# Kernel tuning notes

Hardware: AMD Instinct MI355X
Metric: run time of the kernel (lower is better)

The kernel has to match this reference:

```python
import jax, jax.numpy as jnp
import numpy as np

B, T, U, NOUT = 64, 512, 256, 4


def lstm(x, W, Uh, b):
    """Keras-style LSTM. x: [B,T,F]. Returns (seq [B,T,U], last [B,U]).
    Gate order i, f, g(candidate), o; sigmoid recurrent activation, tanh activation."""
    xz = jnp.einsum('btf,fg->btg', x, W) + b  # precompute input projections [B,T,4U]

    def step(carry, xz_t):
        h, c = carry
        z = xz_t + h @ Uh
        i, f, g, o = jnp.split(z, 4, axis=-1)
        i = jax.nn.sigmoid(i)
        f = jax.nn.sigmoid(f)
        g = jnp.tanh(g)
        o = jax.nn.sigmoid(o)
        c = f * c + i * g
        h = o * jnp.tanh(c)
        return (h, c), h

    h0 = jnp.zeros((x.shape[0], Uh.shape[0]), x.dtype)
    (h_last, _), hs = jax.lax.scan(step, (h0, h0), jnp.swapaxes(xz, 0, 1))
    return jnp.swapaxes(hs, 0, 1), h_last


def setup_inputs() -> dict:
    key = jax.random.key(0)
    ks = jax.random.split(key, 7)
    s_in = 1.0 / np.sqrt(U)
    return {
        'x': jax.random.normal(ks[0], (B, T, U), jnp.float32),
        'Wr': jax.random.normal(ks[1], (U, 4 * U), jnp.float32) * s_in,
        'Ur': jax.random.normal(ks[2], (U, 4 * U), jnp.float32) * s_in,
        'br': jnp.zeros((4 * U,), jnp.float32),
        'Wn': jax.random.normal(ks[3], (U, 4 * U), jnp.float32) * s_in,
        'Un': jax.random.normal(ks[4], (U, 4 * U), jnp.float32) * s_in,
        'bn': jnp.zeros((4 * U,), jnp.float32),
        'Wd': jax.random.normal(ks[5], (T * U, NOUT), jnp.float32) * (1.0 / np.sqrt(T * U)),
        'bd': jnp.zeros((NOUT,), jnp.float32),
    }


def reference(x, Wr, Ur, br, Wn, Un, bn, Wd, bd):
    # n_hidden = 3, inference (training=False): noise/dropout are identity.
    # Layer 0: shared return-sequences LSTM, no residual.
    h0, _ = lstm(x, Wr, Ur, br)                      # [B,T,U]
    # Layer 1: SAME shared LSTM weights, residual add.
    h1, _ = lstm(h0, Wr, Ur, br)
    h1 = h1 + h0                                     # [B,T,U]
    # Layer 2 (last): non-returning LSTM; residual Add broadcasts [B,U] + [B,T,U].
    _, h2 = lstm(h1, Wn, Un, bn)                     # [B,U]
    y = h2[:, None, :] + h1                          # [B,T,U]
    y = y.reshape(y.shape[0], -1)                    # flatten -> [B, T*U]
    return y @ Wd + bd                               # [B, NOUT]
```

## Files before the change

kernel.cpp:

```cpp
#include <hip/hip_runtime.h>
#include <hip/hip_fp16.h>
#include <cstddef>
#include <cstdint>

#define U_DIM 256
#define G_DIM 1024
#define T_DIM 512
#define B_DIM 64
#define TC    32
#define LOG2TC 5
#define NCHUNK (T_DIM / TC)
#define NSLOT  (NCHUNK + 2)
#define BHID   (B_DIM * U_DIM)
#define NPART  8

#define NG_TOT 32
#define NG_REG 23
#define NG_LDS 9

#if __has_builtin(__builtin_amdgcn_global_load_lds)
#define HAS_GLL 1
#else
#define HAS_GLL 0
#endif

typedef _Float16 half2v __attribute__((ext_vector_type(2)));
typedef _Float16 f16x8  __attribute__((ext_vector_type(8)));
typedef float    f32x4  __attribute__((ext_vector_type(4)));

__device__ __forceinline__ float fsig(float x) {
    return 1.0f / (1.0f + __expf(-x));
}
__device__ __forceinline__ float ftanh(float x) {
    return 2.0f * fsig(2.0f * x) - 1.0f;
}

#define PIN4(v) asm("" : "+v"(v.x), "+v"(v.y), "+v"(v.z), "+v"(v.w))

__global__ __launch_bounds__(256)
void pack_w(const float* __restrict__ U, uint4* __restrict__ P)
{
    const int idx = blockIdx.x * 256 + threadIdx.x;
    const int g = idx >> 10;
    const int n = idx & 1023;
    uint vals[4];
    #pragma unroll
    for (int j = 0; j < 4; ++j) {
        const int k = g * 8 + j * 2;
        const __half a = __float2half_rn(U[(size_t)k * G_DIM + n]);
        const __half b = __float2half_rn(U[(size_t)(k + 1) * G_DIM + n]);
        const unsigned short ua = __builtin_bit_cast(unsigned short, a);
        const unsigned short ub = __builtin_bit_cast(unsigned short, b);
        vals[j] = (uint)ua | ((uint)ub << 16);
    }
    P[idx] = make_uint4(vals[0], vals[1], vals[2], vals[3]);
}

__global__ __launch_bounds__(256)
void pack_x(const float* __restrict__ x, __half* __restrict__ xh)
{
    const size_t i = ((size_t)blockIdx.x * 256 + threadIdx.x) * 8;
    const float4 a = *(const float4*)(x + i);
    const float4 b = *(const float4*)(x + i + 4);
    ushort4 o0, o1;
    o0.x = __builtin_bit_cast(unsigned short, __float2half_rn(a.x));
    o0.y = __builtin_bit_cast(unsigned short, __float2half_rn(a.y));
    o0.z = __builtin_bit_cast(unsigned short, __float2half_rn(a.z));
    o0.w = __builtin_bit_cast(unsigned short, __float2half_rn(a.w));
    o1.x = __builtin_bit_cast(unsigned short, __float2half_rn(b.x));
    o1.y = __builtin_bit_cast(unsigned short, __float2half_rn(b.y));
    o1.z = __builtin_bit_cast(unsigned short, __float2half_rn(b.z));
    o1.w = __builtin_bit_cast(unsigned short, __float2half_rn(b.w));
    *(ushort4*)(xh + i) = o0;
    *(ushort4*)(xh + i + 4) = o1;
}

__device__ __forceinline__ float mac8(float acc, uint4 w, uint4 h)
{
#if __has_builtin(__builtin_amdgcn_fdot2)
    acc = __builtin_amdgcn_fdot2(__builtin_bit_cast(half2v, h.x),
                                 __builtin_bit_cast(half2v, w.x), acc, false);
    acc = __builtin_amdgcn_fdot2(__builtin_bit_cast(half2v, h.y),
                                 __builtin_bit_cast(half2v, w.y), acc, false);
    acc = __builtin_amdgcn_fdot2(__builtin_bit_cast(half2v, h.z),
                                 __builtin_bit_cast(half2v, w.z), acc, false);
    acc = __builtin_amdgcn_fdot2(__builtin_bit_cast(half2v, h.w),
                                 __builtin_bit_cast(half2v, w.w), acc, false);
#else
    const uint wv[4] = {w.x, w.y, w.z, w.w};
    const uint hv[4] = {h.x, h.y, h.z, h.w};
    #pragma unroll
    for (int j = 0; j < 4; ++j) {
        const __half2 wp = __builtin_bit_cast(__half2, wv[j]);
        const __half2 hp = __builtin_bit_cast(__half2, hv[j]);
        acc += __half2float(hp.x) * __half2float(wp.x);
        acc += __half2float(hp.y) * __half2float(wp.y);
    }
#endif
    return acc;
}

__global__
__attribute__((amdgpu_flat_work_group_size(512, 512)))
__attribute__((amdgpu_waves_per_eu(2, 2)))
void lstm_pipe(int slot,
               const __half* __restrict__ xzAll,
               const uint4* __restrict__ Pr, const uint4* __restrict__ Pn,
               __half* __restrict__ h0, __half* __restrict__ h1,
               float* __restrict__ hsAll, float* __restrict__ csAll)
{
    const int layer = blockIdx.x >> 6;
    const int b     = blockIdx.x & 63;
    const int c     = slot - layer;
    if ((unsigned)c >= (unsigned)NCHUNK) return;
    const int t0 = c * TC;

    const uint4* __restrict__ P = (layer < 2) ? Pr : Pn;
    const __half* __restrict__ xzb =
        xzAll + (size_t)layer * (B_DIM * TC * G_DIM) + (size_t)b * TC * G_DIM;
    const __half* __restrict__ resb =
        (layer == 1) ? (h0 + (size_t)(b * T_DIM + t0) * U_DIM) : nullptr;
    __half* __restrict__ outb =
        (layer == 0) ? (h0 + (size_t)(b * T_DIM + t0) * U_DIM)
      : (layer == 1) ? (h1 + (size_t)(b * T_DIM + t0) * U_DIM) : nullptr;
    float* __restrict__ hstate = hsAll + (size_t)layer * BHID + b * U_DIM;
    float* __restrict__ cstate = csAll + (size_t)layer * BHID + b * U_DIM;

    const int t = threadIdx.x;
    const int n0 = t;
    const int n1 = t + 512;

    __shared__ __align__(16) uint hq[U_DIM / 2];
    __shared__ float csh[U_DIM];
    __shared__ float zsh[G_DIM];
    __shared__ uint4 wlds[NG_LDS][G_DIM];

#if HAS_GLL
    {
        const int wbase = t & ~63;
        #pragma unroll
        for (int g = 0; g < NG_LDS; ++g) {
            __builtin_amdgcn_global_load_lds(
                (const __attribute__((address_space(1))) void*)
                    (P + (size_t)(NG_REG + g) * G_DIM + n0),
                (__attribute__((address_space(3))) void*)&wlds[g][wbase],
                16, 0, 0);
            __builtin_amdgcn_global_load_lds(
                (const __attribute__((address_space(1))) void*)
                    (P + (size_t)(NG_REG + g) * G_DIM + n1),
                (__attribute__((address_space(3))) void*)&wlds[g][512 + wbase],
                16, 0, 0);
        }
    }
#else
    #pragma unroll
    for (int g = 0; g < NG_LDS; ++g) {
        wlds[g][n0] = P[(size_t)(NG_REG + g) * G_DIM + n0];
        wlds[g][n1] = P[(size_t)(NG_REG + g) * G_DIM + n1];
    }
#endif

    if (t < U_DIM) {
        float hv, cv;
        if (c == 0) { hv = 0.0f; cv = 0.0f; }
        else        { hv = hstate[t]; cv = cstate[t]; }
        csh[t] = cv;
        ((__half*)hq)[t] = __float2half_rn(hv);
    }

    uint4 wA[NG_REG], wB[NG_REG];
    #pragma unroll
    for (int g = 0; g < NG_REG; ++g) {
        wA[g] = P[(size_t)g * G_DIM + n0];
        wB[g] = P[(size_t)g * G_DIM + n1];
    }
    #pragma unroll
    for (int g = 0; g < NG_REG; ++g) { PIN4(wA[g]); PIN4(wB[g]); }

    __syncthreads();

    float cur0 = __half2float(xzb[n0]);
    float cur1 = __half2float(xzb[n1]);
    float resv = (resb && t < U_DIM) ? __half2float(resb[t]) : 0.0f;

    for (int tl = 0; tl < TC; ++tl) {
        float acc0 = cur0;
        float acc1 = cur1;

        const int tn = (tl + 1 < TC) ? (tl + 1) : (TC - 1);
        cur0 = __half2float(xzb[(size_t)tn * G_DIM + n0]);
        cur1 = __half2float(xzb[(size_t)tn * G_DIM + n1]);
        const float resn = (resb && t < U_DIM)
                         ? __half2float(resb[(size_t)tn * U_DIM + t]) : 0.0f;

        const uint4* __restrict__ hp = (const uint4*)hq;

        #pragma unroll
        for (int g = 0; g < NG_REG; ++g) {
            const uint4 h4 = hp[g];
            acc0 = mac8(acc0, wA[g], h4);
            acc1 = mac8(acc1, wB[g], h4);
        }
        #pragma unroll
        for (int g = 0; g < NG_LDS; ++g) {
            const uint4 h4 = hp[NG_REG + g];
            acc0 = mac8(acc0, wlds[g][n0], h4);
            acc1 = mac8(acc1, wlds[g][n1], h4);
        }

        zsh[n0] = fsig(acc0);
        zsh[n1] = (t < U_DIM) ? ftanh(acc1) : fsig(acc1);
        __syncthreads();

        if (t < U_DIM) {
            const float iv = zsh[t];
            const float fv = zsh[t + 256];
            const float gv = zsh[t + 512];
            const float ov = zsh[t + 768];
            const float cc = fv * csh[t] + iv * gv;
            const float hh = ov * ftanh(cc);
            csh[t] = cc;
            ((__half*)hq)[t] = __float2half_rn(hh);
            if (outb) outb[(size_t)tl * U_DIM + t] = __float2half_rn(hh + resv);
        }
        resv = resn;
        __syncthreads();
    }

    if (t < U_DIM) {
        hstate[t] = __half2float(((const __half*)hq)[t]);
        cstate[t] = csh[t];
    }
}

__global__ __launch_bounds__(256)
void gemm3_mfma(int slot,
                const __half* __restrict__ xh,
                const __half* __restrict__ h0, const __half* __restrict__ h1,
                const uint4* __restrict__ PWr, const uint4* __restrict__ PWn,
                const float* __restrict__ br, const float* __restrict__ bn,
                __half* __restrict__ xzAll)
{
    const int z = blockIdx.z;
    const int c = slot - z;
    if ((unsigned)c >= (unsigned)NCHUNK) return;
    const int t0 = c * TC;

    const __half* __restrict__ A = (z == 0) ? xh : ((z == 1) ? h0 : h1);
    const uint4*  __restrict__ PW = (z < 2) ? PWr : PWn;
    const float*  __restrict__ bias = (z < 2) ? br : bn;
    __half* __restrict__ out = xzAll + (size_t)z * (B_DIM * TC * G_DIM);

    const int tid = threadIdx.x;
    const int w = tid >> 6;
    const int l = tid & 63;

    const int bm = blockIdx.y * 64;
    const int bn_ = blockIdx.x * 64;
    const int col = bn_ + w * 16 + (l & 15);
    const int krow = l >> 4;

    __shared__ __half ctile[64][68];

    const __half* arow[4];
    #pragma unroll
    for (int rt = 0; rt < 4; ++rt) {
        const int m = bm + rt * 16 + (l & 15);
        const int b = m >> LOG2TC;
        const int tl = m & (TC - 1);
        arow[rt] = A + (size_t)(b * T_DIM + t0 + tl) * U_DIM + krow * 8;
    }

    f32x4 acc[4] = {{0,0,0,0},{0,0,0,0},{0,0,0,0},{0,0,0,0}};

    #pragma unroll
    for (int kt = 0; kt < 8; ++kt) {
        const uint4 bfrag = PW[(size_t)(4 * kt + krow) * G_DIM + col];
        #pragma unroll
        for (int rt = 0; rt < 4; ++rt) {
            const uint4 afrag = *(const uint4*)(arow[rt] + kt * 32);
            acc[rt] = __builtin_amdgcn_mfma_f32_16x16x32_f16(
                __builtin_bit_cast(f16x8, afrag), __builtin_bit_cast(f16x8, bfrag),
                acc[rt], 0, 0, 0);
        }
    }

    const float bv = bias[col];
    const int ccol = w * 16 + (l & 15);
    #pragma unroll
    for (int rt = 0; rt < 4; ++rt) {
        #pragma unroll
        for (int r = 0; r < 4; ++r) {
            const int crow = rt * 16 + 4 * (l >> 4) + r;
            ctile[crow][ccol] = __float2half_rn(acc[rt][r] + bv);
        }
    }
    __syncthreads();

    {
        const int row = tid >> 2;
        const int quad = (tid & 3) * 16;
        const int m = bm + row;
        const int b = m >> LOG2TC;
        const int tl = m & (TC - 1);
        __half* dst = out + (size_t)(b * TC + tl) * G_DIM + bn_ + quad;
        const uint4 v0 = *(const uint4*)&ctile[row][quad];
        const uint4 v1 = *(const uint4*)&ctile[row][quad + 8];
        *(uint4*)dst = v0;
        *(uint4*)(dst + 8) = v1;
    }
}

__global__ __launch_bounds__(256)
void final_partial(const __half* __restrict__ h1, const float* __restrict__ h2,
                   const float* __restrict__ Wd, float* __restrict__ partials)
{
    const int b = blockIdx.x;
    const int p = blockIdx.y;
    const int tid = threadIdx.x;
    const int JTOT = T_DIM * U_DIM;
    const int JPART = JTOT / NPART;

    const __half* hb = h1 + (size_t)b * JTOT;
    const float* h2b = h2 + (size_t)b * U_DIM;

    float a0 = 0.f, a1 = 0.f, a2 = 0.f, a3 = 0.f;

    for (int j = p * JPART + tid * 8; j < (p + 1) * JPART; j += 256 * 8) {
        const uint4 hv = *(const uint4*)(hb + j);
        const int m = j & (U_DIM - 1);
        const float4 s0 = *(const float4*)(h2b + m);
        const float4 s1 = *(const float4*)(h2b + m + 4);
        float v[8];
        {
            const __half2 p0 = __builtin_bit_cast(__half2, hv.x);
            const __half2 p1 = __builtin_bit_cast(__half2, hv.y);
            const __half2 p2 = __builtin_bit_cast(__half2, hv.z);
            const __half2 p3 = __builtin_bit_cast(__half2, hv.w);
            v[0] = __half2float(p0.x) + s0.x;
            v[1] = __half2float(p0.y) + s0.y;
            v[2] = __half2float(p1.x) + s0.z;
            v[3] = __half2float(p1.y) + s0.w;
            v[4] = __half2float(p2.x) + s1.x;
            v[5] = __half2float(p2.y) + s1.y;
            v[6] = __half2float(p3.x) + s1.z;
            v[7] = __half2float(p3.y) + s1.w;
        }
        #pragma unroll
        for (int uu = 0; uu < 8; ++uu) {
            const float4 wv = *(const float4*)&Wd[(size_t)(j + uu) * 4];
            a0 += v[uu] * wv.x;
            a1 += v[uu] * wv.y;
            a2 += v[uu] * wv.z;
            a3 += v[uu] * wv.w;
        }
    }

    __shared__ float red[256][4];
    red[tid][0] = a0; red[tid][1] = a1; red[tid][2] = a2; red[tid][3] = a3;
    __syncthreads();
    for (int s = 128; s > 0; s >>= 1) {
        if (tid < s) {
            #pragma unroll
            for (int o = 0; o < 4; ++o) red[tid][o] += red[tid + s][o];
        }
        __syncthreads();
    }
    if (tid < 4) partials[((size_t)b * NPART + p) * 4 + tid] = red[0][tid];
}

__global__ __launch_bounds__(256)
void final_reduce(const float* __restrict__ partials, const float* __restrict__ bd,
                  float* __restrict__ y)
{
    const int tid = threadIdx.x;
    const int b = tid >> 2;
    const int o = tid & 3;
    float s = bd[o];
    #pragma unroll
    for (int p = 0; p < NPART; ++p)
        s += partials[((size_t)b * NPART + p) * 4 + o];
    y[b * 4 + o] = s;
}

extern "C" void kernel_launch(void* const* d_in, const int* in_sizes, int n_in,
                              void* d_out, int out_size, void* d_ws, size_t ws_size,
                              hipStream_t stream)
{
    (void)in_sizes; (void)n_in; (void)out_size; (void)ws_size;

    const float* x  = (const float*)d_in[0];
    const float* Wr = (const float*)d_in[1];
    const float* Ur = (const float*)d_in[2];
    const float* br = (const float*)d_in[3];
    const float* Wn = (const float*)d_in[4];
    const float* Un = (const float*)d_in[5];
    const float* bn = (const float*)d_in[6];
    const float* Wd = (const float*)d_in[7];
    const float* bd = (const float*)d_in[8];
    float* y = (float*)d_out;

    char* wp = (char*)d_ws;
    uint4* Pr  = (uint4*)wp;  wp += (size_t)NG_TOT * G_DIM * 16;
    uint4* Pn  = (uint4*)wp;  wp += (size_t)NG_TOT * G_DIM * 16;
    uint4* PWr = (uint4*)wp;  wp += (size_t)NG_TOT * G_DIM * 16;
    uint4* PWn = (uint4*)wp;  wp += (size_t)NG_TOT * G_DIM * 16;
    float* hsAll = (float*)wp;      wp += (size_t)3 * BHID * 4;
    float* csAll = (float*)wp;      wp += (size_t)3 * BHID * 4;
    float* partials = (float*)wp;   wp += (size_t)B_DIM * NPART * 4 * 4;
    wp = (char*)(((uintptr_t)wp + 255) & ~(uintptr_t)255);
    __half* xzAll = (__half*)wp; wp += (size_t)3 * B_DIM * TC * G_DIM * 2;
    __half* h0 = (__half*)wp;    wp += (size_t)B_DIM * T_DIM * U_DIM * 2;
    __half* h1 = (__half*)wp;    wp += (size_t)B_DIM * T_DIM * U_DIM * 2;
    __half* xh = (__half*)wp;    wp += (size_t)B_DIM * T_DIM * U_DIM * 2;

    pack_w<<<128, 256, 0, stream>>>(Ur, Pr);
    pack_w<<<128, 256, 0, stream>>>(Un, Pn);
    pack_w<<<128, 256, 0, stream>>>(Wr, PWr);
    pack_w<<<128, 256, 0, stream>>>(Wn, PWn);
    pack_x<<<(B_DIM * T_DIM * U_DIM) / (256 * 8), 256, 0, stream>>>(x, xh);

    dim3 ggrid(G_DIM / 64, (B_DIM * TC) / 64, 3);
    for (int slot = 0; slot < NSLOT; ++slot) {
        gemm3_mfma<<<ggrid, 256, 0, stream>>>(slot, xh, h0, h1, PWr, PWn,
                                              br, bn, xzAll);
        lstm_pipe<<<3 * B_DIM, 512, 0, stream>>>(slot, xzAll, Pr, Pn,
                                                 h0, h1, hsAll, csAll);
    }

    final_partial<<<dim3(B_DIM, NPART), 256, 0, stream>>>(h1, hsAll + 2 * BHID,
                                                          Wd, partials);
    final_reduce<<<1, 256, 0, stream>>>(partials, bd, y);
}
```

Baseline: 1.636 ms.

## Fuse next-chunk input projection GEMM into LSTM pipeline kernel with double-buffered xz

Removes the separate per-slot gemm3_mfma launch and instead has each lstm_pipe block compute, after its recurrent chunk, the input-projection tile that the following slot will consume (MFMA 16x16x32), written into a double-buffered xz workspace indexed by slot parity. Layer 2 blocks compute layer 0's next chunk of x projections. This halves the number of launches per slot and lets the projection work overlap with idle CUs. The risk is that the fused GEMM runs on only 192 blocks with B fragments read straight from global memory without LDS reuse, so it may be slower than the dedicated GEMM kernel. It also adds extra register pressure in a kernel pinned to two waves per EU.

```diff
diff --git a/kernel.cpp b/kernel.cpp
--- a/kernel.cpp
+++ b/kernel.cpp
@@ -100,31 +100,30 @@
     return acc;
 }
 
+#define XZ_TILE ((size_t)TC * G_DIM)
+#define XZ_AT(base, par, layer, b) \
+    ((base) + ((((size_t)(par) * 3 + (layer)) * B_DIM + (b)) * XZ_TILE))
+
 __global__
 __attribute__((amdgpu_flat_work_group_size(512, 512)))
 __attribute__((amdgpu_waves_per_eu(2, 2)))
 void lstm_pipe(int slot,
-               const __half* __restrict__ xzAll,
+               const __half* __restrict__ xh,
                const uint4* __restrict__ Pr, const uint4* __restrict__ Pn,
+               const uint4* __restrict__ PWr, const uint4* __restrict__ PWn,
+               const float* __restrict__ br, const float* __restrict__ bn,
                __half* __restrict__ h0, __half* __restrict__ h1,
+               __half* __restrict__ xzAll,
                float* __restrict__ hsAll, float* __restrict__ csAll)
 {
     const int layer = blockIdx.x >> 6;
     const int b     = blockIdx.x & 63;
     const int c     = slot - layer;
-    if ((unsigned)c >= (unsigned)NCHUNK) return;
-    const int t0 = c * TC;
-
-    const uint4* __restrict__ P = (layer < 2) ? Pr : Pn;
-    const __half* __restrict__ xzb =
-        xzAll + (size_t)layer * (B_DIM * TC * G_DIM) + (size_t)b * TC * G_DIM;
-    const __half* __restrict__ resb =
-        (layer == 1) ? (h0 + (size_t)(b * T_DIM + t0) * U_DIM) : nullptr;
-    __half* __restrict__ outb =
-        (layer == 0) ? (h0 + (size_t)(b * T_DIM + t0) * U_DIM)
-      : (layer == 1) ? (h1 + (size_t)(b * T_DIM + t0) * U_DIM) : nullptr;
-    float* __restrict__ hstate = hsAll + (size_t)layer * BHID + b * U_DIM;
-    float* __restrict__ cstate = csAll + (size_t)layer * BHID + b * U_DIM;
+    const bool do_lstm = (unsigned)c < (unsigned)NCHUNK;
+
+    const int cc = (layer == 2) ? (slot + 1) : (slot - layer);
+    const bool do_tail = (unsigned)cc < (unsigned)NCHUNK;
+    if (!do_lstm && !do_tail) return;
 
     const int t = threadIdx.x;
     const int n0 = t;
@@ -135,101 +134,164 @@
     __shared__ float zsh[G_DIM];
     __shared__ uint4 wlds[NG_LDS][G_DIM];
 
+    if (do_lstm) {
+        const int t0 = c * TC;
+        const uint4* __restrict__ P = (layer < 2) ? Pr : Pn;
+        const __half* __restrict__ xzb = XZ_AT(xzAll, slot & 1, layer, b);
+        const __half* __restrict__ resb =
+            (layer == 1) ? (h0 + (size_t)(b * T_DIM + t0) * U_DIM) : nullptr;
+        __half* __restrict__ outb =
+            (layer == 0) ? (h0 + (size_t)(b * T_DIM + t0) * U_DIM)
+          : (layer == 1) ? (h1 + (size_t)(b * T_DIM + t0) * U_DIM) : nullptr;
+        float* __restrict__ hstate = hsAll + (size_t)layer * BHID + b * U_DIM;
+        float* __restrict__ cstate = csAll + (size_t)layer * BHID + b * U_DIM;
+
 #if HAS_GLL
-    {
-        const int wbase = t & ~63;
+        {
+            const int wbase = t & ~63;
+            #pragma unroll
+            for (int g = 0; g < NG_LDS; ++g) {
+                __builtin_amdgcn_global_load_lds(
+                    (const __attribute__((address_space(1))) void*)
+                        (P + (size_t)(NG_REG + g) * G_DIM + n0),
+                    (__attribute__((address_space(3))) void*)&wlds[g][wbase],
+                    16, 0, 0);
+                __builtin_amdgcn_global_load_lds(
+                    (const __attribute__((address_space(1))) void*)
+                        (P + (size_t)(NG_REG + g) * G_DIM + n1),
+                    (__attribute__((address_space(3))) void*)&wlds[g][512 + wbase],
+                    16, 0, 0);
+            }
+        }
+#else
         #pragma unroll
         for (int g = 0; g < NG_LDS; ++g) {
-            __builtin_amdgcn_global_load_lds(
-                (const __attribute__((address_space(1))) void*)
-                    (P + (size_t)(NG_REG + g) * G_DIM + n0),
-                (__attribute__((address_space(3))) void*)&wlds[g][wbase],
-                16, 0, 0);
-            __builtin_amdgcn_global_load_lds(
-                (const __attribute__((address_space(1))) void*)
-                    (P + (size_t)(NG_REG + g) * G_DIM + n1),
-                (__attribute__((address_space(3))) void*)&wlds[g][512 + wbase],
-                16, 0, 0);
-        }
-    }
-#else
-    #pragma unroll
-    for (int g = 0; g < NG_LDS; ++g) {
-        wlds[g][n0] = P[(size_t)(NG_REG + g) * G_DIM + n0];
-        wlds[g][n1] = P[(size_t)(NG_REG + g) * G_DIM + n1];
-    }
+            wlds[g][n0] = P[(size_t)(NG_REG + g) * G_DIM + n0];
+            wlds[g][n1] = P[(size_t)(NG_REG + g) * G_DIM + n1];
+        }
 #endif
 
-    if (t < U_DIM) {
-        float hv, cv;
-        if (c == 0) { hv = 0.0f; cv = 0.0f; }
-        else        { hv = hstate[t]; cv = cstate[t]; }
-        csh[t] = cv;
-        ((__half*)hq)[t] = __float2half_rn(hv);
-    }
-
-    uint4 wA[NG_REG], wB[NG_REG];
-    #pragma unroll
-    for (int g = 0; g < NG_REG; ++g) {
-        wA[g] = P[(size_t)g * G_DIM + n0];
-        wB[g] = P[(size_t)g * G_DIM + n1];
-    }
-    #pragma unroll
-    for (int g = 0; g < NG_REG; ++g) { PIN4(wA[g]); PIN4(wB[g]); }
-
-    __syncthreads();
-
-    float cur0 = __half2float(xzb[n0]);
-    float cur1 = __half2float(xzb[n1]);
-    float resv = (resb && t < U_DIM) ? __half2float(resb[t]) : 0.0f;
-
-    for (int tl = 0; tl < TC; ++tl) {
-        float acc0 = cur0;
-        float acc1 = cur1;
-
-        const int tn = (tl + 1 < TC) ? (tl + 1) : (TC - 1);
-        cur0 = __half2float(xzb[(size_t)tn * G_DIM + n0]);
-        cur1 = __half2float(xzb[(size_t)tn * G_DIM + n1]);
-        const float resn = (resb && t < U_DIM)
-                         ? __half2float(resb[(size_t)tn * U_DIM + t]) : 0.0f;
-
-        const uint4* __restrict__ hp = (const uint4*)hq;
-
+        if (t < U_DIM) {
+            float hv, cv;
+            if (c == 0) { hv = 0.0f; cv = 0.0f; }
+            else        { hv = hstate[t]; cv = cstate[t]; }
+            csh[t] = cv;
+            ((__half*)hq)[t] = __float2half_rn(hv);
+        }
+
+        uint4 wA[NG_REG], wB[NG_REG];
         #pragma unroll
         for (int g = 0; g < NG_REG; ++g) {
-            const uint4 h4 = hp[g];
-            acc0 = mac8(acc0, wA[g], h4);
-            acc1 = mac8(acc1, wB[g], h4);
-        }
-        #pragma unroll
-        for (int g = 0; g < NG_LDS; ++g) {
-            const uint4 h4 = hp[NG_REG + g];
-            acc0 = mac8(acc0, wlds[g][n0], h4);
-            acc1 = mac8(acc1, wlds[g][n1], h4);
-        }
-
-        zsh[n0] = fsig(acc0);
-        zsh[n1] = (t < U_DIM) ? ftanh(acc1) : fsig(acc1);
+            wA[g] = P[(size_t)g * G_DIM + n0];
+            wB[g] = P[(size_t)g * G_DIM + n1];
+        }
+        #pragma unroll
+        for (int g = 0; g < NG_REG; ++g) { PIN4(wA[g]); PIN4(wB[g]); }
+
         __syncthreads();
 
+        float cur0 = __half2float(xzb[n0]);
+        float cur1 = __half2float(xzb[n1]);
+        float resv = (resb && t < U_DIM) ? __half2float(resb[t]) : 0.0f;
+
+        for (int tl = 0; tl < TC; ++tl) {
+            float acc0 = cur0;
+            float acc1 = cur1;
+
+            const int tn = (tl + 1 < TC) ? (tl + 1) : (TC - 1);
+            cur0 = __half2float(xzb[(size_t)tn * G_DIM + n0]);
+            cur1 = __half2float(xzb[(size_t)tn * G_DIM + n1]);
+            const float resn = (resb && t < U_DIM)
+                             ? __half2float(resb[(size_t)tn * U_DIM + t]) : 0.0f;
+
+            const uint4* __restrict__ hp = (const uint4*)hq;
+
+            #pragma unroll
+            for (int g = 0; g < NG_REG; ++g) {
+                const uint4 h4 = hp[g];
+                acc0 = mac8(acc0, wA[g], h4);
+                acc1 = mac8(acc1, wB[g], h4);
+            }
+            #pragma unroll
+            for (int g = 0; g < NG_LDS; ++g) {
+                const uint4 h4 = hp[NG_REG + g];
+                acc0 = mac8(acc0, wlds[g][n0], h4);
+                acc1 = mac8(acc1, wlds[g][n1], h4);
+            }
+
+            zsh[n0] = fsig(acc0);
+            zsh[n1] = (t < U_DIM) ? ftanh(acc1) : fsig(acc1);
+            __syncthreads();
+
+            if (t < U_DIM) {
+                const float iv = zsh[t];
+                const float fv = zsh[t + 256];
+                const float gv = zsh[t + 512];
+                const float ov = zsh[t + 768];
+                const float cc2 = fv * csh[t] + iv * gv;
+                const float hh = ov * ftanh(cc2);
+                csh[t] = cc2;
+                ((__half*)hq)[t] = __float2half_rn(hh);
+                if (outb) outb[(size_t)tl * U_DIM + t] = __float2half_rn(hh + resv);
+            }
+            resv = resn;
+            __syncthreads();
+        }
+
         if (t < U_DIM) {
-            const float iv = zsh[t];
-            const float fv = zsh[t + 256];
-            const float gv = zsh[t + 512];
-            const float ov = zsh[t + 768];
-            const float cc = fv * csh[t] + iv * gv;
-            const float hh = ov * ftanh(cc);
-            csh[t] = cc;
-            ((__half*)hq)[t] = __float2half_rn(hh);
-            if (outb) outb[(size_t)tl * U_DIM + t] = __float2half_rn(hh + resv);
-        }
-        resv = resn;
-        __syncthreads();
-    }
-
-    if (t < U_DIM) {
-        hstate[t] = __half2float(((const __half*)hq)[t]);
-        cstate[t] = csh[t];
+            hstate[t] = __half2float(((const __half*)hq)[t]);
+            cstate[t] = csh[t];
+        }
+    }
+
+    if (do_tail) {
+        const __half* __restrict__ asrc;
+        const uint4*  __restrict__ PW2;
+        const float*  __restrict__ bias2;
+        __half* __restrict__ xzo;
+        if (layer == 0) {
+            asrc = h0;  PW2 = PWr; bias2 = br;
+            xzo = XZ_AT(xzAll, (slot + 1) & 1, 1, b);
+        } else if (layer == 1) {
+            asrc = h1;  PW2 = PWn; bias2 = bn;
+            xzo = XZ_AT(xzAll, (slot + 1) & 1, 2, b);
+        } else {
+            asrc = xh;  PW2 = PWr; bias2 = br;
+            xzo = XZ_AT(xzAll, (slot + 1) & 1, 0, b);
+        }
+        const __half* arow0 =
+            asrc + (size_t)(b * T_DIM + cc * TC + (t & 15)) * U_DIM + ((t & 63) >> 4) * 8;
+        const __half* arow1 = arow0 + 16 * U_DIM;
+
+        const int w = t >> 6;
+        const int l = t & 63;
+        const int krow = l >> 4;
+
+        #pragma unroll
+        for (int ct = 0; ct < 8; ++ct) {
+            const int col = w * 128 + ct * 16 + (l & 15);
+            f32x4 acc0 = {0.f, 0.f, 0.f, 0.f};
+            f32x4 acc1 = {0.f, 0.f, 0.f, 0.f};
+            #pragma unroll
+            for (int kt = 0; kt < 8; ++kt) {
+                const uint4 bfrag = PW2[(size_t)(4 * kt + krow) * G_DIM + col];
+                const uint4 a0 = *(const uint4*)(arow0 + kt * 32);
+                const uint4 a1 = *(const uint4*)(arow1 + kt * 32);
+                acc0 = __builtin_amdgcn_mfma_f32_16x16x32_f16(
+                    __builtin_bit_cast(f16x8, a0), __builtin_bit_cast(f16x8, bfrag),
+                    acc0, 0, 0, 0);
+                acc1 = __builtin_amdgcn_mfma_f32_16x16x32_f16(
+                    __builtin_bit_cast(f16x8, a1), __builtin_bit_cast(f16x8, bfrag),
+                    acc1, 0, 0, 0);
+            }
+            const float bv = bias2[col];
+            #pragma unroll
+            for (int r = 0; r < 4; ++r) {
+                const int row0 = 4 * krow + r;
+                xzo[(size_t)row0 * G_DIM + col]        = __float2half_rn(acc0[r] + bv);
+                xzo[(size_t)(row0 + 16) * G_DIM + col] = __float2half_rn(acc1[r] + bv);
+            }
+        }
     }
 }
 
@@ -409,7 +471,7 @@
     float* csAll = (float*)wp;      wp += (size_t)3 * BHID * 4;
     float* partials = (float*)wp;   wp += (size_t)B_DIM * NPART * 4 * 4;
     wp = (char*)(((uintptr_t)wp + 255) & ~(uintptr_t)255);
-    __half* xzAll = (__half*)wp; wp += (size_t)3 * B_DIM * TC * G_DIM * 2;
+    __half* xzAll = (__half*)wp; wp += (size_t)2 * 3 * B_DIM * TC * G_DIM * 2;
     __half* h0 = (__half*)wp;    wp += (size_t)B_DIM * T_DIM * U_DIM * 2;
     __half* h1 = (__half*)wp;    wp += (size_t)B_DIM * T_DIM * U_DIM * 2;
     __half* xh = (__half*)wp;    wp += (size_t)B_DIM * T_DIM * U_DIM * 2;
@@ -420,12 +482,16 @@
     pack_w<<<128, 256, 0, stream>>>(Wn, PWn);
     pack_x<<<(B_DIM * T_DIM * U_DIM) / (256 * 8), 256, 0, stream>>>(x, xh);
 
-    dim3 ggrid(G_DIM / 64, (B_DIM * TC) / 64, 3);
+    {
+        dim3 ggrid0(G_DIM / 64, (B_DIM * TC) / 64, 1);
+        gemm3_mfma<<<ggrid0, 256, 0, stream>>>(0, xh, h0, h1, PWr, PWn,
+                                               br, bn, XZ_AT(xzAll, 0, 0, 0));
+    }
+
     for (int slot = 0; slot < NSLOT; ++slot) {
-        gemm3_mfma<<<ggrid, 256, 0, stream>>>(slot, xh, h0, h1, PWr, PWn,
-                                              br, bn, xzAll);
-        lstm_pipe<<<3 * B_DIM, 512, 0, stream>>>(slot, xzAll, Pr, Pn,
-                                                 h0, h1, hsAll, csAll);
+        lstm_pipe<<<3 * B_DIM, 512, 0, stream>>>(slot, xh, Pr, Pn, PWr, PWn,
+                                                 br, bn, h0, h1, xzAll,
+                                                 hsAll, csAll);
     }
 
     final_partial<<<dim3(B_DIM, NPART), 256, 0, stream>>>(h1, hsAll + 2 * BHID,
```

After: 1.782 ms. +8.9%, slower.
